# Kernel optimization log

Hardware: AMD Instinct MI355X
Metric: run time of the kernel (lower is better)

The kernel has to match this reference:

```python
import jax, jax.numpy as jnp
import numpy as np

N_NODES = 50000
N_EDGES = 600000
D_FT = 128   # prompt_dim == node feature dim
D_E = 32     # edge feature dim


def setup_inputs() -> dict:
    key = jax.random.key(0)
    k1, k2, k3, k4, k5 = jax.random.split(key, 5)
    graph_embedding = jax.random.normal(k1, (N_NODES, D_FT), dtype=jnp.float32)
    e_feat = jax.random.normal(k2, (N_EDGES, D_E), dtype=jnp.float32)
    weight = jax.random.normal(k3, (1, D_FT), dtype=jnp.float32)  # learned prompt
    src_idx = jax.random.randint(k4, (N_EDGES,), 0, N_NODES)
    dst_idx = jax.random.randint(k5, (N_EDGES,), 0, N_NODES)
    return {"graph_embedding": graph_embedding, "e_feat": e_feat,
            "weight": weight, "src_idx": src_idx, "dst_idx": dst_idx}


def reference(graph_embedding, e_feat, weight, src_idx, dst_idx):
    # message m = concat(src_ft * p, e); dst_ft = segment_sum(m over dst).
    # concat commutes with segment-sum, so reduce the two halves separately
    # and concatenate at node level (avoids materializing [E, D_FT+D_E]).
    src_ft = graph_embedding[src_idx] * weight            # [E, D_FT]
    agg_ft = jax.ops.segment_sum(src_ft, dst_idx, num_segments=N_NODES)
    agg_e = jax.ops.segment_sum(e_feat, dst_idx, num_segments=N_NODES)
    return jnp.concatenate([agg_ft, agg_e], axis=1)      # [N, D_FT+D_E]
```

## Files before the change

### kernel.cpp

```cpp
#include <hip/hip_runtime.h>


#define D_FT 128
#define D_E 32
#define D_OUT (D_FT + D_E)
#define CAP 32

__global__ void place_bucket_kernel(const int* __restrict__ src_idx,
                                    const int* __restrict__ dst_idx,
                                    int* __restrict__ cursor,
                                    int2* __restrict__ bucket,
                                    int* __restrict__ ovf,
                                    int* __restrict__ ovf_cnt, int E) {
    int i = blockIdx.x * blockDim.x + threadIdx.x;
    if (i >= E) return;
    int d = dst_idx[i];
    int slot = atomicAdd(&cursor[d], 1);
    if (slot < CAP) {
        int2 pr; pr.x = src_idx[i]; pr.y = i;
        bucket[(size_t)d * CAP + slot] = pr;
    } else {
        int p = atomicAdd(ovf_cnt, 1);
        ovf[p] = i;
    }
}

__global__ void gather_bucket_kernel(const float* __restrict__ emb,
                                     const float* __restrict__ e_feat,
                                     const float* __restrict__ w,
                                     const int* __restrict__ cursor,
                                     const int2* __restrict__ bucket,
                                     float* __restrict__ out, int N) {
    int g = (blockIdx.x * blockDim.x + threadIdx.x) >> 5;
    if (g >= N) return;
    const int q  = threadIdx.x & 31;
    const int qg = q >> 3;
    const int ql = q & 7;
    int cnt = cursor[g];
    cnt = cnt > CAP ? CAP : cnt;
    int2 pr = make_int2(0, 0);
    if (q < cnt) pr = bucket[(size_t)g * CAP + q];

    float4 accft = make_float4(0.f, 0.f, 0.f, 0.f);
    float4 acce  = make_float4(0.f, 0.f, 0.f, 0.f);

    int i = 0;
    for (; i + 4 <= cnt; i += 4) {
        int s0 = __shfl(pr.x, i + 0, 32);
        int s1 = __shfl(pr.x, i + 1, 32);
        int s2 = __shfl(pr.x, i + 2, 32);
        int s3 = __shfl(pr.x, i + 3, 32);
        int ee = __shfl(pr.y, i + qg, 32);
        float4 v0 = *reinterpret_cast<const float4*>(emb + (size_t)s0 * D_FT + q * 4);
        float4 v1 = *reinterpret_cast<const float4*>(emb + (size_t)s1 * D_FT + q * 4);
        float4 v2 = *reinterpret_cast<const float4*>(emb + (size_t)s2 * D_FT + q * 4);
        float4 v3 = *reinterpret_cast<const float4*>(emb + (size_t)s3 * D_FT + q * 4);
        float4 a  = *reinterpret_cast<const float4*>(e_feat + (size_t)ee * D_E + ql * 4);
        accft.x += (v0.x + v1.x) + (v2.x + v3.x);
        accft.y += (v0.y + v1.y) + (v2.y + v3.y);
        accft.z += (v0.z + v1.z) + (v2.z + v3.z);
        accft.w += (v0.w + v1.w) + (v2.w + v3.w);
        acce.x += a.x; acce.y += a.y; acce.z += a.z; acce.w += a.w;
    }
    {
        int t = i + qg;
        int tsrc = (t < cnt) ? t : 0;
        int ee = __shfl(pr.y, tsrc, 32);
        if (t < cnt) {
            float4 a = *reinterpret_cast<const float4*>(e_feat + (size_t)ee * D_E + ql * 4);
            acce.x += a.x; acce.y += a.y; acce.z += a.z; acce.w += a.w;
        }
    }
    for (int j = i; j < cnt; ++j) {
        int s = __shfl(pr.x, j, 32);
        float4 v = *reinterpret_cast<const float4*>(emb + (size_t)s * D_FT + q * 4);
        accft.x += v.x; accft.y += v.y; accft.z += v.z; accft.w += v.w;
    }

    acce.x += __shfl_xor(acce.x, 8, 32);
    acce.y += __shfl_xor(acce.y, 8, 32);
    acce.z += __shfl_xor(acce.z, 8, 32);
    acce.w += __shfl_xor(acce.w, 8, 32);
    acce.x += __shfl_xor(acce.x, 16, 32);
    acce.y += __shfl_xor(acce.y, 16, 32);
    acce.z += __shfl_xor(acce.z, 16, 32);
    acce.w += __shfl_xor(acce.w, 16, 32);

    float4 wv = *reinterpret_cast<const float4*>(w + q * 4);
    float* o = out + (size_t)g * D_OUT;
    *reinterpret_cast<float4*>(o + q * 4) =
        make_float4(accft.x * wv.x, accft.y * wv.y, accft.z * wv.z, accft.w * wv.w);
    if (q < 8)
        *reinterpret_cast<float4*>(o + D_FT + q * 4) = acce;
}

__global__ void ovf_scatter_kernel(const float* __restrict__ emb,
                                   const float* __restrict__ e_feat,
                                   const float* __restrict__ w,
                                   const int* __restrict__ src_idx,
                                   const int* __restrict__ dst_idx,
                                   const int* __restrict__ ovf,
                                   const int* __restrict__ ovf_cnt,
                                   float* __restrict__ out) {
    int n = *ovf_cnt;
    int total = n * 40;
    for (int t = blockIdx.x * blockDim.x + threadIdx.x; t < total;
         t += gridDim.x * blockDim.x) {
        int e = t / 40, slot = t % 40;
        int eid = ovf[e];
        int d = dst_idx[eid];
        float* o = out + (size_t)d * D_OUT;
        if (slot < 32) {
            int s = src_idx[eid];
            float4 v  = *reinterpret_cast<const float4*>(emb + (size_t)s * D_FT + slot * 4);
            float4 wv = *reinterpret_cast<const float4*>(w + slot * 4);
            atomicAdd(o + slot * 4 + 0, v.x * wv.x);
            atomicAdd(o + slot * 4 + 1, v.y * wv.y);
            atomicAdd(o + slot * 4 + 2, v.z * wv.z);
            atomicAdd(o + slot * 4 + 3, v.w * wv.w);
        } else {
            int qq = slot - 32;
            float4 ve = *reinterpret_cast<const float4*>(e_feat + (size_t)eid * D_E + qq * 4);
            atomicAdd(o + D_FT + qq * 4 + 0, ve.x);
            atomicAdd(o + D_FT + qq * 4 + 1, ve.y);
            atomicAdd(o + D_FT + qq * 4 + 2, ve.z);
            atomicAdd(o + D_FT + qq * 4 + 3, ve.w);
        }
    }
}

__global__ void scatter_ft_kernel(const float* __restrict__ emb, const float* __restrict__ w,
                                  const int* __restrict__ src_idx, const int* __restrict__ dst_idx,
                                  float* __restrict__ out, int n_items) {
    int idx = blockIdx.x * blockDim.x + threadIdx.x;
    if (idx >= n_items) return;
    int e = idx >> 5, q = idx & 31;
    int s = src_idx[e], d = dst_idx[e];
    const float4 v  = *reinterpret_cast<const float4*>(emb + (size_t)s * D_FT + q * 4);
    const float4 wv = *reinterpret_cast<const float4*>(w + q * 4);
    float* o = out + (size_t)d * D_OUT + q * 4;
    atomicAdd(o + 0, v.x * wv.x); atomicAdd(o + 1, v.y * wv.y);
    atomicAdd(o + 2, v.z * wv.z); atomicAdd(o + 3, v.w * wv.w);
}
__global__ void scatter_e_kernel(const float* __restrict__ e_feat, const int* __restrict__ dst_idx,
                                 float* __restrict__ out, int n_items) {
    int idx = blockIdx.x * blockDim.x + threadIdx.x;
    if (idx >= n_items) return;
    int e = idx >> 3, q = idx & 7;
    int d = dst_idx[e];
    const float4 v = *reinterpret_cast<const float4*>(e_feat + (size_t)e * D_E + q * 4);
    float* o = out + (size_t)d * D_OUT + D_FT + q * 4;
    atomicAdd(o + 0, v.x); atomicAdd(o + 1, v.y);
    atomicAdd(o + 2, v.z); atomicAdd(o + 3, v.w);
}

extern "C" void kernel_launch(void* const* d_in, const int* in_sizes, int n_in,
                              void* d_out, int out_size, void* d_ws, size_t ws_size,
                              hipStream_t stream) {
    const float* emb    = (const float*)d_in[0];
    const float* e_feat = (const float*)d_in[1];
    const float* w      = (const float*)d_in[2];
    const int*   src    = (const int*)d_in[3];
    const int*   dst    = (const int*)d_in[4];
    float* out = (float*)d_out;

    const int E = in_sizes[3];
    const int N = out_size / D_OUT;

    size_t ints_head = (size_t)N + 2;
    size_t need = ints_head * 4 + (size_t)N * CAP * 8 + (size_t)E * 4;

    if (ws_size >= need) {
        int*  cursor  = (int*)d_ws;
        int*  ovf_cnt = cursor + N;
        int2* bucket  = (int2*)(cursor + ints_head);
        int*  ovf     = (int*)(bucket + (size_t)N * CAP);

        hipMemsetAsync(cursor, 0, ints_head * sizeof(int), stream);
        place_bucket_kernel<<<(E + 255) / 256, 256, 0, stream>>>(
            src, dst, cursor, bucket, ovf, ovf_cnt, E);
        gather_bucket_kernel<<<((size_t)N * 32 + 255) / 256, 256, 0, stream>>>(
            emb, e_feat, w, cursor, bucket, out, N);
        ovf_scatter_kernel<<<128, 256, 0, stream>>>(
            emb, e_feat, w, src, dst, ovf, ovf_cnt, out);
    } else {
        hipMemsetAsync(d_out, 0, (size_t)out_size * sizeof(float), stream);
        int items_ft = E * 32, items_e = E * 8;
        scatter_ft_kernel<<<(items_ft + 255) / 256, 256, 0, stream>>>(emb, w, src, dst, out, items_ft);
        scatter_e_kernel<<<(items_e + 255) / 256, 256, 0, stream>>>(e_feat, dst, out, items_e);
    }
}
```

Before: 103.2 us.

## Use full 64-lane wavefront per node in gather and add nontemporal loads/stores

The gather kernel now assigns a full 64-lane wavefront to each destination node instead of 32 lanes. The two half-waves process alternate groups of four edges and are combined with cross-half shuffle reductions. Bucket reads, edge-feature reads and output writes use nontemporal builtins to reduce cache pollution. This doubles the number of threads launched and adds reduction shuffles, while aiming for more memory parallelism per node given the average in-degree of about 12.

```diff
diff --git a/kernel.cpp b/kernel.cpp
--- a/kernel.cpp
+++ b/kernel.cpp
@@ -6,10 +6,13 @@
 #define D_OUT (D_FT + D_E)
 #define CAP 32
 
+typedef float f32x4 __attribute__((ext_vector_type(4)));
+typedef int   i32x2 __attribute__((ext_vector_type(2)));
+
 __global__ void place_bucket_kernel(const int* __restrict__ src_idx,
                                     const int* __restrict__ dst_idx,
                                     int* __restrict__ cursor,
-                                    int2* __restrict__ bucket,
+                                    i32x2* __restrict__ bucket,
                                     int* __restrict__ ovf,
                                     int* __restrict__ ovf_cnt, int E) {
     int i = blockIdx.x * blockDim.x + threadIdx.x;
@@ -17,7 +20,7 @@
     int d = dst_idx[i];
     int slot = atomicAdd(&cursor[d], 1);
     if (slot < CAP) {
-        int2 pr; pr.x = src_idx[i]; pr.y = i;
+        i32x2 pr; pr.x = src_idx[i]; pr.y = i;
         bucket[(size_t)d * CAP + slot] = pr;
     } else {
         int p = atomicAdd(ovf_cnt, 1);
@@ -29,33 +32,39 @@
                                      const float* __restrict__ e_feat,
                                      const float* __restrict__ w,
                                      const int* __restrict__ cursor,
-                                     const int2* __restrict__ bucket,
+                                     const i32x2* __restrict__ bucket,
                                      float* __restrict__ out, int N) {
-    int g = (blockIdx.x * blockDim.x + threadIdx.x) >> 5;
+    int g = (blockIdx.x * blockDim.x + threadIdx.x) >> 6;
     if (g >= N) return;
-    const int q  = threadIdx.x & 31;
-    const int qg = q >> 3;
-    const int ql = q & 7;
+    const int lane = threadIdx.x & 63;
+    const int half = lane >> 5;
+    const int q    = lane & 31;
+    const int qg   = q >> 3;
+    const int ql   = q & 7;
+
     int cnt = cursor[g];
     cnt = cnt > CAP ? CAP : cnt;
-    int2 pr = make_int2(0, 0);
-    if (q < cnt) pr = bucket[(size_t)g * CAP + q];
+    i32x2 pr; pr.x = 0; pr.y = 0;
+    if (lane < cnt)
+        pr = __builtin_nontemporal_load(&bucket[(size_t)g * CAP + lane]);
 
     float4 accft = make_float4(0.f, 0.f, 0.f, 0.f);
     float4 acce  = make_float4(0.f, 0.f, 0.f, 0.f);
 
     int i = 0;
-    for (; i + 4 <= cnt; i += 4) {
-        int s0 = __shfl(pr.x, i + 0, 32);
-        int s1 = __shfl(pr.x, i + 1, 32);
-        int s2 = __shfl(pr.x, i + 2, 32);
-        int s3 = __shfl(pr.x, i + 3, 32);
-        int ee = __shfl(pr.y, i + qg, 32);
+    for (; i + 8 <= cnt; i += 8) {
+        int b  = i + (half << 2);
+        int s0 = __shfl(pr.x, b + 0, 64);
+        int s1 = __shfl(pr.x, b + 1, 64);
+        int s2 = __shfl(pr.x, b + 2, 64);
+        int s3 = __shfl(pr.x, b + 3, 64);
+        int ee = __shfl(pr.y, b + qg, 64);
         float4 v0 = *reinterpret_cast<const float4*>(emb + (size_t)s0 * D_FT + q * 4);
         float4 v1 = *reinterpret_cast<const float4*>(emb + (size_t)s1 * D_FT + q * 4);
         float4 v2 = *reinterpret_cast<const float4*>(emb + (size_t)s2 * D_FT + q * 4);
         float4 v3 = *reinterpret_cast<const float4*>(emb + (size_t)s3 * D_FT + q * 4);
-        float4 a  = *reinterpret_cast<const float4*>(e_feat + (size_t)ee * D_E + ql * 4);
+        f32x4 a = __builtin_nontemporal_load(
+            reinterpret_cast<const f32x4*>(e_feat + (size_t)ee * D_E + ql * 4));
         accft.x += (v0.x + v1.x) + (v2.x + v3.x);
         accft.y += (v0.y + v1.y) + (v2.y + v3.y);
         accft.z += (v0.z + v1.z) + (v2.z + v3.z);
@@ -63,35 +72,53 @@
         acce.x += a.x; acce.y += a.y; acce.z += a.z; acce.w += a.w;
     }
     {
-        int t = i + qg;
+        int t = i + (half << 2) + qg;
         int tsrc = (t < cnt) ? t : 0;
-        int ee = __shfl(pr.y, tsrc, 32);
+        int ee = __shfl(pr.y, tsrc, 64);
         if (t < cnt) {
-            float4 a = *reinterpret_cast<const float4*>(e_feat + (size_t)ee * D_E + ql * 4);
+            f32x4 a = __builtin_nontemporal_load(
+                reinterpret_cast<const f32x4*>(e_feat + (size_t)ee * D_E + ql * 4));
             acce.x += a.x; acce.y += a.y; acce.z += a.z; acce.w += a.w;
         }
     }
-    for (int j = i; j < cnt; ++j) {
-        int s = __shfl(pr.x, j, 32);
-        float4 v = *reinterpret_cast<const float4*>(emb + (size_t)s * D_FT + q * 4);
-        accft.x += v.x; accft.y += v.y; accft.z += v.z; accft.w += v.w;
-    }
-
-    acce.x += __shfl_xor(acce.x, 8, 32);
-    acce.y += __shfl_xor(acce.y, 8, 32);
-    acce.z += __shfl_xor(acce.z, 8, 32);
-    acce.w += __shfl_xor(acce.w, 8, 32);
-    acce.x += __shfl_xor(acce.x, 16, 32);
-    acce.y += __shfl_xor(acce.y, 16, 32);
-    acce.z += __shfl_xor(acce.z, 16, 32);
-    acce.w += __shfl_xor(acce.w, 16, 32);
-
-    float4 wv = *reinterpret_cast<const float4*>(w + q * 4);
-    float* o = out + (size_t)g * D_OUT;
-    *reinterpret_cast<float4*>(o + q * 4) =
-        make_float4(accft.x * wv.x, accft.y * wv.y, accft.z * wv.z, accft.w * wv.w);
-    if (q < 8)
-        *reinterpret_cast<float4*>(o + D_FT + q * 4) = acce;
+    for (int j = i; j < cnt; j += 2) {
+        int t = j + half;
+        int tsrc = (t < cnt) ? t : 0;
+        int s = __shfl(pr.x, tsrc, 64);
+        if (t < cnt) {
+            float4 v = *reinterpret_cast<const float4*>(emb + (size_t)s * D_FT + q * 4);
+            accft.x += v.x; accft.y += v.y; accft.z += v.z; accft.w += v.w;
+        }
+    }
+
+    accft.x += __shfl_xor(accft.x, 32, 64);
+    accft.y += __shfl_xor(accft.y, 32, 64);
+    accft.z += __shfl_xor(accft.z, 32, 64);
+    accft.w += __shfl_xor(accft.w, 32, 64);
+    acce.x += __shfl_xor(acce.x, 8, 64);
+    acce.y += __shfl_xor(acce.y, 8, 64);
+    acce.z += __shfl_xor(acce.z, 8, 64);
+    acce.w += __shfl_xor(acce.w, 8, 64);
+    acce.x += __shfl_xor(acce.x, 16, 64);
+    acce.y += __shfl_xor(acce.y, 16, 64);
+    acce.z += __shfl_xor(acce.z, 16, 64);
+    acce.w += __shfl_xor(acce.w, 16, 64);
+    acce.x += __shfl_xor(acce.x, 32, 64);
+    acce.y += __shfl_xor(acce.y, 32, 64);
+    acce.z += __shfl_xor(acce.z, 32, 64);
+    acce.w += __shfl_xor(acce.w, 32, 64);
+
+    if (half == 0) {
+        float4 wv = *reinterpret_cast<const float4*>(w + q * 4);
+        float* o = out + (size_t)g * D_OUT;
+        f32x4 r; r.x = accft.x * wv.x; r.y = accft.y * wv.y;
+                 r.z = accft.z * wv.z; r.w = accft.w * wv.w;
+        __builtin_nontemporal_store(r, reinterpret_cast<f32x4*>(o + q * 4));
+        if (q < 8) {
+            f32x4 re; re.x = acce.x; re.y = acce.y; re.z = acce.z; re.w = acce.w;
+            __builtin_nontemporal_store(re, reinterpret_cast<f32x4*>(o + D_FT + q * 4));
+        }
+    }
 }
 
 __global__ void ovf_scatter_kernel(const float* __restrict__ emb,
@@ -171,15 +198,15 @@
     size_t need = ints_head * 4 + (size_t)N * CAP * 8 + (size_t)E * 4;
 
     if (ws_size >= need) {
-        int*  cursor  = (int*)d_ws;
-        int*  ovf_cnt = cursor + N;
-        int2* bucket  = (int2*)(cursor + ints_head);
-        int*  ovf     = (int*)(bucket + (size_t)N * CAP);
+        int*   cursor  = (int*)d_ws;
+        int*   ovf_cnt = cursor + N;
+        i32x2* bucket  = (i32x2*)(cursor + ints_head);
+        int*   ovf     = (int*)(bucket + (size_t)N * CAP);
 
         hipMemsetAsync(cursor, 0, ints_head * sizeof(int), stream);
         place_bucket_kernel<<<(E + 255) / 256, 256, 0, stream>>>(
             src, dst, cursor, bucket, ovf, ovf_cnt, E);
-        gather_bucket_kernel<<<((size_t)N * 32 + 255) / 256, 256, 0, stream>>>(
+        gather_bucket_kernel<<<((size_t)N * 64 + 255) / 256, 256, 0, stream>>>(
             emb, e_feat, w, cursor, bucket, out, N);
         ovf_scatter_kernel<<<128, 256, 0, stream>>>(
             emb, e_feat, w, src, dst, ovf, ovf_cnt, out);
```

Result: no change. 103.2 us (+0.1%).
